# Optimization experiments

Measured on AMD Instinct MI355X. Metric: run time of the kernel, lower is better.

Reference implementation:

```python
import jax, jax.numpy as jnp
import numpy as np
from jax import lax

EQN = 10  # equations per pixel in FlowLayer


def build_a(h, w):
    """Dense constraint basis a[num, EQN, 4*num] (<=2 nonzeros per row), as in FlowLayer.__init__."""
    num = h * w
    a = np.zeros((num, EQN, 4 * num), np.float32)
    for i in range(num):
        right = (i + 1) % w != 0 and i + 1 < num
        down = i + w < num
        if right:
            a[i, 0, 2 * num + i] = 1.0; a[i, 0, i + 1] = -1.0
            a[i, 2, 2 * num + i] = 1.0; a[i, 2, 2 * num + i + 1] = -1.0
            a[i, 4, i] = 1.0;           a[i, 4, i + 1] = -1.0
            a[i, 6, 3 * num + i] = 1.0; a[i, 6, 3 * num + i + 1] = -1.0
            a[i, 8, num + i] = 1.0;     a[i, 8, num + i + 1] = -1.0
        if down:
            a[i, 1, 3 * num + i] = 1.0; a[i, 1, num + i + w] = -1.0
            a[i, 3, 3 * num + i] = 1.0; a[i, 3, 3 * num + i + w] = -1.0
            a[i, 5, num + i] = 1.0;     a[i, 5, num + i + w] = -1.0
            a[i, 7, 2 * num + i] = 1.0; a[i, 7, 2 * num + i + w] = -1.0
            a[i, 9, i] = 1.0;           a[i, 9, i + w] = -1.0
    last = num - 1  # anchor equations for the last pixel
    a[last, 0, 2 * num + last] = 1.0
    a[last, 1, 3 * num + last] = 1.0
    a[last, 2, 2 * num + last] = 1.0
    a[last, 3, 3 * num + last] = 1.0
    a[last, 4, last] = 1.0
    a[last, 5, num + last] = 1.0
    a[last, 6, 3 * num + last] = 1.0
    a[last, 7, 2 * num + last] = 1.0
    a[last, 8, num + last] = 1.0
    a[last, 9, last] = 1.0
    return a


def conv2d(x, w, b):
    y = lax.conv_general_dilated(x, w, (1, 1), 'SAME',
                                 dimension_numbers=('NCHW', 'OIHW', 'NCHW'))
    return y + b[None, :, None, None]


def setup_inputs() -> dict:
    key = jax.random.key(0)
    N, C, H, W, GR = 4, 64, 16, 16, 4
    ks = jax.random.split(key, 12)
    s3, s1 = 0.04, 0.1  # ~1/sqrt(fan_in) scales
    inp = {
        'x': jax.random.normal(ks[0], (N, C, H, W), jnp.float32),
        'grad_w1': jax.random.normal(ks[1], (C, C, 3, 3), jnp.float32) * s3,
        'grad_b1': jnp.zeros((C,), jnp.float32),
        'grad_w2': jax.random.normal(ks[2], (EQN * GR, C, 3, 3), jnp.float32) * s3,
        'grad_b2': jnp.zeros((EQN * GR,), jnp.float32),
        'att_w1': jax.random.normal(ks[3], (C, C, 3, 3), jnp.float32) * s3,
        'att_b1': jnp.zeros((C,), jnp.float32),
        'att_w2': jax.random.normal(ks[4], (EQN * GR, C, 3, 3), jnp.float32) * s3,
        'att_b2': jnp.zeros((EQN * GR,), jnp.float32),
        'se_w1': jax.random.normal(ks[5], (C // 2, C, 1, 1), jnp.float32) * s1,
        'se_b1': jnp.zeros((C // 2,), jnp.float32),
        'se_w2': jax.random.normal(ks[6], (4 * GR, C // 2, 1, 1), jnp.float32) * s1,
        'se_b2': jnp.zeros((4 * GR,), jnp.float32),
        'gn_w': jnp.ones((4 * GR,), jnp.float32),
        'gn_b': jnp.zeros((4 * GR,), jnp.float32),
        'post_w': jax.random.normal(ks[7], (128, 4 * GR, 3, 3), jnp.float32) * s1,
        'post_b': jnp.zeros((128,), jnp.float32),
    }
    return inp


def reference(x, grad_w1, grad_b1, grad_w2, grad_b2,
              att_w1, att_b1, att_w2, att_b2,
              se_w1, se_b1, se_w2, se_b2,
              gn_w, gn_b, post_w, post_b):
    n, c, h, w = x.shape
    gr = gn_w.shape[0] // 4
    num = h * w
    lrelu = lambda t: jax.nn.leaky_relu(t, 0.01)

    grad = conv2d(lrelu(conv2d(x, grad_w1, grad_b1)), grad_w2, grad_b2)      # [n, eqn*gr, h, w]
    att = jax.nn.sigmoid(conv2d(lrelu(conv2d(x, att_w1, att_b1)), att_w2, att_b2))
    pooled = x.mean((2, 3), keepdims=True)                                     # AdaptiveAvgPool2d(1)
    se = jax.nn.sigmoid(conv2d(lrelu(conv2d(pooled, se_w1, se_b1)), se_w2, se_b2))  # [n, 4*gr, 1, 1]

    # reshape(n*gr, EQN, hw).permute -> [B, hw, EQN] -> flatten rows as (pixel, eqn)
    att_f = att.reshape(n * gr, EQN, num).transpose(0, 2, 1).reshape(n * gr, num * EQN)
    grad_f = grad.reshape(n * gr, EQN, num).transpose(0, 2, 1).reshape(n * gr, num * EQN)

    a_flat = jnp.asarray(build_a(h, w)).reshape(num * EQN, 4 * num)  # constant basis
    A = att_f[:, :, None] * a_flat[None]                 # [B, num*EQN, 4*num]
    b_vec = att_f * grad_f                               # [B, num*EQN]
    ATA = jnp.einsum('brj,brk->bjk', A, A)               # [B, 4num, 4num]
    ATB = jnp.einsum('brj,br->bj', A, b_vec)[..., None]  # [B, 4num, 1]
    jitter = jnp.eye(4 * num, dtype=x.dtype) * 1e-12
    sol = jnp.linalg.solve(ATA + jitter[None], ATB)      # [B, 4num, 1]

    y = sol.reshape(n, 4 * gr, h, w)
    # GroupNorm(1, 4*gr): normalize over (C,H,W) per sample
    mu = y.mean((1, 2, 3), keepdims=True)
    var = ((y - mu) ** 2).mean((1, 2, 3), keepdims=True)
    y = (y - mu) / jnp.sqrt(var + 1e-5)
    y = y * gn_w[None, :, None, None] + gn_b[None, :, None, None]
    y = se * y
    return conv2d(y, post_w, post_b)  # [n, 128, h, w]
```

## Files before the change

### kernel.cpp

```cpp
#include <hip/hip_runtime.h>

#define NCHEB 8

typedef __attribute__((ext_vector_type(8))) short vs8;
typedef __attribute__((ext_vector_type(4))) float vf4;
typedef __attribute__((ext_vector_type(16))) float vf16;

__device__ __forceinline__ unsigned short f2bf(float f) {
  union { float f; unsigned int u; } x; x.f = f;
  unsigned int r = (x.u + 0x7FFFu + ((x.u >> 16) & 1u)) >> 16;
  return (unsigned short)r;
}

template<int COUT, int TILES, bool SE>
__global__ __launch_bounds__(256) void k_conv(
    const float* __restrict__ inA, const float* __restrict__ inB,
    const float* __restrict__ wA, const float* __restrict__ bA,
    const float* __restrict__ wB, const float* __restrict__ bB,
    float* __restrict__ outA, float* __restrict__ outB,
    int actA, int actB,
    const float* __restrict__ x,
    const float* __restrict__ sw1, const float* __restrict__ sb1,
    const float* __restrict__ sw2, const float* __restrict__ sb2,
    float* __restrict__ seo) {
  __shared__ unsigned short Xl[256 * 64];
  __shared__ unsigned short Wl[9 * 16 * 64];
  __shared__ float sp[64];
  __shared__ float sh1[32];
  const int b = blockIdx.x;
  const int t = threadIdx.x;

  if (SE && b >= 8 * TILES) {
    const int n = b - 8 * TILES;
    const int c = t >> 2, part = t & 3;
    const float* xp = x + (n * 64 + c) * 256 + part * 64;
    float s = 0.f;
    for (int k = 0; k < 64; ++k) s += xp[k];
    s += __shfl_xor(s, 1, 64);
    s += __shfl_xor(s, 2, 64);
    if (part == 0) sp[c] = s * (1.f / 256.f);
    __syncthreads();
    if (t < 32) {
      float a = sb1[t];
      for (int k = 0; k < 64; ++k) a += sw1[t * 64 + k] * sp[k];
      sh1[t] = a > 0.f ? a : 0.01f * a;
    }
    __syncthreads();
    if (t < 16) {
      float a = sb2[t];
      for (int k = 0; k < 32; ++k) a += sw2[t * 32 + k] * sh1[k];
      seo[n * 16 + t] = 1.f / (1.f + __expf(-a));
    }
    return;
  }

  const int n = b & 3;
  const int q = b >> 2;
  const int br = (q >= TILES) ? 1 : 0;
  const int ct = q - br * TILES;
  const int co0 = ct * 16;
  const float* inp = (br ? inB : inA) + n * 64 * 256;
  const float* wsrc = br ? wB : wA;
  const float* bias = br ? bB : bA;
  float* outp = (br ? outB : outA) + n * COUT * 256;
  const int act = br ? actB : actA;

  {
    const int p = t;
    #pragma unroll
    for (int q8 = 0; q8 < 8; ++q8) {
      vs8 v;
      #pragma unroll
      for (int j = 0; j < 8; ++j) v[j] = (short)f2bf(inp[(8 * q8 + j) * 256 + p]);
      *(vs8*)&Xl[p * 64 + ((q8 ^ (p & 7)) << 3)] = v;
    }
  }
  {
    const int col = t >> 4;
    const int sub = t & 15;
    const int co = co0 + col;
    if (co < COUT) {
      const float* wp = wsrc + (co * 64 + sub * 4) * 9;
      #pragma unroll
      for (int cc = 0; cc < 4; ++cc) {
        const int ci = sub * 4 + cc;
        #pragma unroll
        for (int e = 0; e < 9; ++e)
          Wl[(e * 16 + col) * 64 + (ci ^ ((col & 7) << 3))] = f2bf(wp[cc * 9 + e]);
      }
    } else {
      #pragma unroll
      for (int cc = 0; cc < 4; ++cc) {
        const int ci = sub * 4 + cc;
        #pragma unroll
        for (int e = 0; e < 9; ++e)
          Wl[(e * 16 + col) * 64 + (ci ^ ((col & 7) << 3))] = 0;
      }
    }
  }
  __syncthreads();

  const int w = t >> 6, lane = t & 63;
  const int px = lane & 15, kg = lane >> 4;
  vf4 acc[4];
  #pragma unroll
  for (int mt = 0; mt < 4; ++mt) acc[mt] = (vf4)0.f;

  for (int e = 0; e < 9; ++e) {
    const int dy = e / 3 - 1, dx = e % 3 - 1;
    const bool xok = (dx == 0) || (dx < 0 ? (px > 0) : (px < 15));
    const int xoff = xok ? dx : 0;
    #pragma unroll
    for (int ks = 0; ks < 2; ++ks) {
      vs8 bf = *(const vs8*)&Wl[(e * 16 + px) * 64 + (((ks * 4 + kg) ^ (px & 7)) << 3)];
      #pragma unroll
      for (int mt = 0; mt < 4; ++mt) {
        const int yy = 4 * w + mt + dy;
        if (yy < 0 || yy > 15) continue;
        const int ps = yy * 16 + px + xoff;
        vs8 a = *(const vs8*)&Xl[ps * 64 + (((ks * 4 + kg) ^ (ps & 7)) << 3)];
        if (!xok) a = (vs8)(short)0;
        acc[mt] = __builtin_amdgcn_mfma_f32_16x16x32_bf16(a, bf, acc[mt], 0, 0, 0);
      }
    }
  }

  const int co = co0 + px;
  if (co < COUT) {
    const float bv = bias[co];
    #pragma unroll
    for (int mt = 0; mt < 4; ++mt) {
      const int y = 4 * w + mt;
      vf4 v = acc[mt];
      #pragma unroll
      for (int j = 0; j < 4; ++j) {
        float s = v[j] + bv;
        if (act == 1) s = s > 0.f ? s : 0.01f * s;
        else if (act == 2) s = 1.f / (1.f + __expf(-s));
        v[j] = s;
      }
      *(vf4*)&outp[co * 256 + y * 16 + kg * 4] = v;
    }
  }
}

__global__ __launch_bounds__(512) void k_post(
    const float* __restrict__ sol, const float* __restrict__ se,
    const float* __restrict__ gn_w, const float* __restrict__ gn_b,
    const float* __restrict__ pw, const float* __restrict__ pb,
    float* __restrict__ out) {
  __shared__ unsigned short Hl[256 * 24];
  __shared__ unsigned short Wp[9 * 128 * 24];
  __shared__ float rs[8];
  __shared__ float rs2[8];
  const int n = blockIdx.x;
  const int t = threadIdx.x;
  const int w = t >> 6, lane = t & 63;

  float v[8];
  {
    const vf4* s4 = (const vf4*)(sol + n * 4096 + 8 * t);
    vf4 a = s4[0], b = s4[1];
    v[0]=a[0];v[1]=a[1];v[2]=a[2];v[3]=a[3];v[4]=b[0];v[5]=b[1];v[6]=b[2];v[7]=b[3];
  }
  float s = 0.f, s2 = 0.f;
  #pragma unroll
  for (int k = 0; k < 8; ++k) { s += v[k]; s2 += v[k] * v[k]; }
  #pragma unroll
  for (int o = 1; o <= 32; o <<= 1) { s += __shfl_xor(s, o, 64); s2 += __shfl_xor(s2, o, 64); }
  if (lane == 0) { rs[w] = s; rs2[w] = s2; }

  {
    const int co = t >> 2, sub = t & 3;
    const float* wp0 = pw + (co * 16 + sub * 4) * 9;
    #pragma unroll
    for (int cc = 0; cc < 4; ++cc) {
      const int ci = sub * 4 + cc;
      #pragma unroll
      for (int e = 0; e < 9; ++e)
        Wp[(e * 128 + co) * 24 + ci] = f2bf(wp0[cc * 9 + e]);
    }
  }
  __syncthreads();
  float sm = 0.f, sq = 0.f;
  #pragma unroll
  for (int k = 0; k < 8; ++k) { sm += rs[k]; sq += rs2[k]; }
  const float mu = sm * (1.f / 4096.f);
  const float rstd = rsqrtf(sq * (1.f / 4096.f) - mu * mu + 1e-5f);

  const int c = t >> 5;
  const int p0 = (8 * t) & 255;
  const float sev = se[n * 16 + c];
  const float sc = rstd * gn_w[c] * sev;
  const float of = (gn_b[c] - mu * rstd * gn_w[c]) * sev;
  #pragma unroll
  for (int k = 0; k < 8; ++k) Hl[(p0 + k) * 24 + c] = f2bf(v[k] * sc + of);
  __syncthreads();

  const int cl = lane & 31, h = lane >> 5;
  const int px = cl & 15, y0 = 2 * w + (cl >> 4);
  vf16 acc[4];
  #pragma unroll
  for (int nt = 0; nt < 4; ++nt) acc[nt] = (vf16)0.f;
  for (int e = 0; e < 9; ++e) {
    const int dy = e / 3 - 1, dx = e % 3 - 1;
    const int yy = y0 + dy, xx = px + dx;
    const bool ok = (yy >= 0 && yy < 16 && xx >= 0 && xx < 16);
    const int ps = ok ? yy * 16 + xx : 0;
    vs8 a = *(const vs8*)&Hl[ps * 24 + h * 8];
    if (!ok) a = (vs8)(short)0;
    #pragma unroll
    for (int nt = 0; nt < 4; ++nt) {
      vs8 bf = *(const vs8*)&Wp[(e * 128 + nt * 32 + cl) * 24 + h * 8];
      acc[nt] = __builtin_amdgcn_mfma_f32_32x32x16_bf16(a, bf, acc[nt], 0, 0, 0);
    }
  }
  float* op = out + n * 32768;
  #pragma unroll
  for (int nt = 0; nt < 4; ++nt) {
    const int co = nt * 32 + cl;
    const float bv = pb[co];
    #pragma unroll
    for (int rq = 0; rq < 4; ++rq) {
      vf4 vv;
      #pragma unroll
      for (int j = 0; j < 4; ++j) vv[j] = acc[nt][rq * 4 + j] + bv;
      *(vf4*)&op[co * 256 + 32 * w + 8 * rq + 4 * h] = vv;
    }
  }
}

__global__ __launch_bounds__(64) void k_pcg(
    const float* __restrict__ att, const float* __restrict__ grad,
    float* __restrict__ sol, int maxit, float tol2) {
  const int sys = blockIdx.x >> 1;
  const int wv = blockIdx.x & 1;
  const int l = threadIdx.x;
  const int row = l >> 2, c4 = l & 3;
  const int i0 = 4 * l;

  const int n = sys >> 2, g = sys & 3;
  const float* ab = att + (n * 40 + g * 10) * 256;
  const float* gb = grad + (n * 40 + g * 10) * 256;

  int era, eda, erb, edb, ec, fa, fb;
  if (wv == 0) { fa = 0; fb = 2; era = 4; eda = 9; erb = 2; edb = 7; ec = 0; }
  else         { fa = 1; fb = 3; era = 8; eda = 5; erb = 6; edb = 3; ec = 1; }

  auto L4 = [](const float* p) { return *reinterpret_cast<const float4*>(p); };
  auto unp = [](float4 v, float* o) { o[0] = v.x; o[1] = v.y; o[2] = v.z; o[3] = v.w; };

  float wLa[4], wRa[4], wUa[4], wDa[4], wXa[4], dga[4], iva[4], rsa[4];
  float wLb[4], wRb[4], wUb[4], wDb[4], wXb[4], dgb[4], ivb[4], rsb[4];

  float rA[4], gA[4], dA[4], hA[4], uA[4] = {0,0,0,0}, vA[4] = {0,0,0,0};
  unp(L4(ab + era * 256 + i0), rA); unp(L4(gb + era * 256 + i0), gA);
  unp(L4(ab + eda * 256 + i0), dA); unp(L4(gb + eda * 256 + i0), hA);
  if (row > 0) { unp(L4(ab + eda * 256 + i0 - 16), uA); unp(L4(gb + eda * 256 + i0 - 16), vA); }
  float rlA = (l > 0) ? ab[era * 256 + i0 - 1] : 0.f;
  float glA = (l > 0) ? gb[era * 256 + i0 - 1] : 0.f;
  float cX[4], gX[4], cU[4] = {0,0,0,0}, gU[4] = {0,0,0,0};
  unp(L4(ab + ec * 256 + i0), cX); unp(L4(gb + ec * 256 + i0), gX);
  float clX = 0.f, glX = 0.f;
  if (wv == 0) { if (l > 0) { clX = ab[ec * 256 + i0 - 1]; glX = gb[ec * 256 + i0 - 1]; } }
  else if (row > 0) { unp(L4(ab + ec * 256 + i0 - 16), cU); unp(L4(gb + ec * 256 + i0 - 16), gU); }

  #pragma unroll
  for (int k = 0; k < 4; ++k) {
    wRa[k] = (k < 3 || c4 < 3) ? rA[k] * rA[k] : 0.f;
    wLa[k] = (k > 0) ? rA[k-1] * rA[k-1] : ((c4 > 0) ? rlA * rlA : 0.f);
    wDa[k] = (row < 15) ? dA[k] * dA[k] : 0.f;
    wUa[k] = (row > 0) ? uA[k] * uA[k] : 0.f;
    float rhs = wRa[k] * gA[k] - wLa[k] * ((k > 0) ? gA[k-1] : glA)
              + wDa[k] * hA[k] - wUa[k] * vA[k];
    float wx, gx;
    if (wv == 0) {
      wx = (k > 0) ? cX[k-1] * cX[k-1] : ((c4 > 0) ? clX * clX : 0.f);
      gx = (k > 0) ? gX[k-1] : glX;
    } else {
      wx = (row > 0) ? cU[k] * cU[k] : 0.f;
      gx = gU[k];
    }
    wXa[k] = wx;
    rhs -= wx * gx;
    rsa[k] = rhs;
    dga[k] = 1e-12f + wRa[k] + wLa[k] + wDa[k] + wUa[k] + wx;
  }

  float rB[4], gB[4], dB[4], hB[4], uB[4] = {0,0,0,0}, vB[4] = {0,0,0,0};
  unp(L4(ab + erb * 256 + i0), rB); unp(L4(gb + erb * 256 + i0), gB);
  unp(L4(ab + edb * 256 + i0), dB); unp(L4(gb + edb * 256 + i0), hB);
  if (row > 0) { unp(L4(ab + edb * 256 + i0 - 16), uB); unp(L4(gb + edb * 256 + i0 - 16), vB); }
  float rlB = (l > 0) ? ab[erb * 256 + i0 - 1] : 0.f;
  float glB = (l > 0) ? gb[erb * 256 + i0 - 1] : 0.f;

  #pragma unroll
  for (int k = 0; k < 4; ++k) {
    wRb[k] = (k < 3 || c4 < 3) ? rB[k] * rB[k] : 0.f;
    wLb[k] = (k > 0) ? rB[k-1] * rB[k-1] : ((c4 > 0) ? rlB * rlB : 0.f);
    wDb[k] = (row < 15) ? dB[k] * dB[k] : 0.f;
    wUb[k] = (row > 0) ? uB[k] * uB[k] : 0.f;
    float wx;
    if (wv == 0) wx = (k < 3 || c4 < 3) ? cX[k] * cX[k] : 0.f;
    else         wx = (row < 15) ? cX[k] * cX[k] : 0.f;
    wXb[k] = wx;
    rsb[k] = wRb[k] * gB[k] - wLb[k] * ((k > 0) ? gB[k-1] : glB)
           + wDb[k] * hB[k] - wUb[k] * vB[k]
           + wx * gX[k];
    dgb[k] = 1e-12f + wRb[k] + wLb[k] + wDb[k] + wUb[k] + wx;
  }

  if (l == 63) {
    float wr = rA[3] * rA[3], wd = dA[3] * dA[3];
    dga[3] += wr + wd;
    rsa[3] += wr * gA[3] + wd * hA[3];
    float wc = cX[3] * cX[3], wrb = rB[3] * rB[3], wdb = dB[3] * dB[3];
    dgb[3] += wc + wrb + wdb;
    rsb[3] += wc * gX[3] + wrb * gB[3] + wdb * hB[3];
  }
  #pragma unroll
  for (int k = 0; k < 4; ++k) { iva[k] = 1.f / dga[k]; ivb[k] = 1.f / dgb[k]; }

  float ua[4], ub[4], wa[4], wb[4];

  auto spmv = [&](const float (&ia_)[4], const float (&ib_)[4],
                  float (&oa)[4], float (&ob)[4]) {
    float aU[4], aD[4], bU[4], bD[4];
    #pragma unroll
    for (int k = 0; k < 4; ++k) {
      aU[k] = __shfl_up(ia_[k], 4, 64);
      aD[k] = __shfl_down(ia_[k], 4, 64);
      bU[k] = __shfl_up(ib_[k], 4, 64);
      bD[k] = __shfl_down(ib_[k], 4, 64);
    }
    float aL = __shfl_up(ia_[3], 1, 64);
    float aR = __shfl_down(ia_[0], 1, 64);
    float bL = __shfl_up(ib_[3], 1, 64);
    float bR = __shfl_down(ib_[0], 1, 64);
    float uaL[4] = {aL, ia_[0], ia_[1], ia_[2]};
    float uaR[4] = {ia_[1], ia_[2], ia_[3], aR};
    float ubL[4] = {bL, ib_[0], ib_[1], ib_[2]};
    float ubR[4] = {ib_[1], ib_[2], ib_[3], bR};
    #pragma unroll
    for (int k = 0; k < 4; ++k) {
      float cA = (wv == 0) ? ubL[k] : bU[k];
      float cB = (wv == 0) ? uaR[k] : aD[k];
      oa[k] = dga[k] * ia_[k] - wLa[k] * uaL[k] - wRa[k] * uaR[k]
            - wUa[k] * aU[k] - wDa[k] * aD[k] - wXa[k] * cA;
      ob[k] = dgb[k] * ib_[k] - wLb[k] * ubL[k] - wRb[k] * ubR[k]
            - wUb[k] * bU[k] - wDb[k] * bD[k] - wXb[k] * cB;
    }
  };

  constexpr float lo = 0.01f, hi = 2.0f;
  constexpr float th = (hi + lo) * 0.5f, dl = (hi - lo) * 0.5f, s1 = th / dl;

  float xa[4] = {0,0,0,0}, xb[4] = {0,0,0,0};
  float ra_[4], rb_[4], pa[4] = {0,0,0,0}, pb_[4] = {0,0,0,0};
  float sa[4] = {0,0,0,0}, sb[4] = {0,0,0,0};
  #pragma unroll
  for (int k = 0; k < 4; ++k) { ra_[k] = rsa[k]; rb_[k] = rsb[k]; }

  auto cheb = [&]() {
    float da_[4], db_[4], ta[4], tb[4], qa[4], qb[4];
    #pragma unroll
    for (int k = 0; k < 4; ++k) {
      da_[k] = (1.0f / th) * iva[k] * ra_[k];
      db_[k] = (1.0f / th) * ivb[k] * rb_[k];
      ua[k] = da_[k]; ub[k] = db_[k];
    }
    spmv(da_, db_, ta, tb);
    #pragma unroll
    for (int k = 0; k < 4; ++k) {
      wa[k] = ta[k]; wb[k] = tb[k];
      qa[k] = ra_[k] - ta[k]; qb[k] = rb_[k] - tb[k];
    }
    float rho = 1.0f / s1;
    #pragma unroll
    for (int j = 1; j < NCHEB; ++j) {
      float rho2 = 1.0f / (2.0f * s1 - rho);
      float c1 = rho2 * rho, c2 = 2.0f * rho2 / dl;
      #pragma unroll
      for (int k = 0; k < 4; ++k) {
        da_[k] = c1 * da_[k] + c2 * iva[k] * qa[k];
        db_[k] = c1 * db_[k] + c2 * ivb[k] * qb[k];
        ua[k] += da_[k]; ub[k] += db_[k];
      }
      spmv(da_, db_, ta, tb);
      #pragma unroll
      for (int k = 0; k < 4; ++k) {
        wa[k] += ta[k]; wb[k] += tb[k];
        qa[k] -= ta[k]; qb[k] -= tb[k];
      }
      rho = rho2;
    }
  };

  float gamma, delta;
  auto dots = [&]() {
    float gp = 0.f, dp = 0.f;
    #pragma unroll
    for (int k = 0; k < 4; ++k) {
      gp += ra_[k] * ua[k] + rb_[k] * ub[k];
      dp += wa[k] * ua[k] + wb[k] * ub[k];
    }
    #pragma unroll
    for (int o = 1; o <= 32; o <<= 1) {
      gp += __shfl_xor(gp, o, 64);
      dp += __shfl_xor(dp, o, 64);
    }
    gamma = gp; delta = dp;
  };

  cheb();
  dots();
  const float thresh = tol2 * gamma;
  float gamma_old = gamma, alpha_old = 1.f;

  for (int it = 0; it < maxit && gamma > thresh; ++it) {
    float beta = (it == 0) ? 0.f : gamma / gamma_old;
    float alpha = (it == 0) ? gamma / delta
                            : gamma / (delta - beta * gamma / alpha_old);
    #pragma unroll
    for (int k = 0; k < 4; ++k) {
      pa[k] = ua[k] + beta * pa[k];   pb_[k] = ub[k] + beta * pb_[k];
      sa[k] = wa[k] + beta * sa[k];   sb[k] = wb[k] + beta * sb[k];
      xa[k] += alpha * pa[k];         xb[k] += alpha * pb_[k];
      ra_[k] -= alpha * sa[k];        rb_[k] -= alpha * sb[k];
    }
    gamma_old = gamma; alpha_old = alpha;
    cheb();
    dots();
  }

  float4* sol4 = reinterpret_cast<float4*>(sol);
  sol4[sys * 256 + fa * 64 + l] = make_float4(xa[0], xa[1], xa[2], xa[3]);
  sol4[sys * 256 + fb * 64 + l] = make_float4(xb[0], xb[1], xb[2], xb[3]);
}

extern "C" void kernel_launch(void* const* d_in, const int* in_sizes, int n_in,
                              void* d_out, int out_size, void* d_ws, size_t ws_size,
                              hipStream_t stream) {
  const float* x       = (const float*)d_in[0];
  const float* grad_w1 = (const float*)d_in[1];
  const float* grad_b1 = (const float*)d_in[2];
  const float* grad_w2 = (const float*)d_in[3];
  const float* grad_b2 = (const float*)d_in[4];
  const float* att_w1  = (const float*)d_in[5];
  const float* att_b1  = (const float*)d_in[6];
  const float* att_w2  = (const float*)d_in[7];
  const float* att_b2  = (const float*)d_in[8];
  const float* se_w1   = (const float*)d_in[9];
  const float* se_b1   = (const float*)d_in[10];
  const float* se_w2   = (const float*)d_in[11];
  const float* se_b2   = (const float*)d_in[12];
  const float* gn_w    = (const float*)d_in[13];
  const float* gn_b    = (const float*)d_in[14];
  const float* post_w  = (const float*)d_in[15];
  const float* post_b  = (const float*)d_in[16];
  float* out = (float*)d_out;
  float* ws = (float*)d_ws;

  float* t1    = ws;
  float* t2    = ws + 65536;
  float* gradb = ws + 131072;
  float* attb  = ws + 172032;
  float* seb   = ws + 212992;
  float* solb  = ws;

  k_conv<64, 4, true><<<36, 256, 0, stream>>>(
      x, x, grad_w1, grad_b1, att_w1, att_b1, t1, t2, 1, 1,
      x, se_w1, se_b1, se_w2, se_b2, seb);
  k_conv<40, 3, false><<<24, 256, 0, stream>>>(
      t1, t2, grad_w2, grad_b2, att_w2, att_b2, gradb, attb, 0, 2,
      nullptr, nullptr, nullptr, nullptr, nullptr, nullptr);
  k_pcg<<<32, 64, 0, stream>>>(attb, gradb, solb, 100, 3e-6f);
  k_post<<<4, 512, 0, stream>>>(solb, seb, gn_w, gn_b, post_w, post_b, out);
}
```

Measured before the change: 68.31 us.

## Fuse four launches into two kernels: front conv chain and PCG+post

Merges the two conv stages and the SE branch into one kernel per (image, branch) that keeps the intermediate activation in LDS as bf16. It also folds the PCG solve into the GroupNorm/post-conv kernel, passing the solution through shared memory. The goal is to remove two launches and the global round trips for the intermediates. In exchange, the first stage now runs on only 8 blocks (down from 36), with serial output-channel tiles and repeated weight reloads, which greatly reduces parallelism across the GPU.

```diff
diff --git a/kernel.cpp b/kernel.cpp
--- a/kernel.cpp
+++ b/kernel.cpp
@@ -12,33 +12,48 @@
   return (unsigned short)r;
 }
 
-template<int COUT, int TILES, bool SE>
-__global__ __launch_bounds__(256) void k_conv(
-    const float* __restrict__ inA, const float* __restrict__ inB,
-    const float* __restrict__ wA, const float* __restrict__ bA,
-    const float* __restrict__ wB, const float* __restrict__ bB,
-    float* __restrict__ outA, float* __restrict__ outB,
-    int actA, int actB,
+__global__ __launch_bounds__(512) void k_front(
     const float* __restrict__ x,
+    const float* __restrict__ w1g, const float* __restrict__ b1g,
+    const float* __restrict__ w1a, const float* __restrict__ b1a,
+    const float* __restrict__ w2g, const float* __restrict__ b2g,
+    const float* __restrict__ w2a, const float* __restrict__ b2a,
     const float* __restrict__ sw1, const float* __restrict__ sb1,
     const float* __restrict__ sw2, const float* __restrict__ sb2,
-    float* __restrict__ seo) {
+    float* __restrict__ grad, float* __restrict__ att,
+    float* __restrict__ seb) {
   __shared__ unsigned short Xl[256 * 64];
-  __shared__ unsigned short Wl[9 * 16 * 64];
+  __shared__ unsigned short Yl[256 * 64];
+  __shared__ unsigned short Wt[9 * 16 * 64];
   __shared__ float sp[64];
   __shared__ float sh1[32];
-  const int b = blockIdx.x;
+  const int br = blockIdx.x & 1;
+  const int n = blockIdx.x >> 1;
   const int t = threadIdx.x;
-
-  if (SE && b >= 8 * TILES) {
-    const int n = b - 8 * TILES;
-    const int c = t >> 2, part = t & 3;
-    const float* xp = x + (n * 64 + c) * 256 + part * 64;
-    float s = 0.f;
-    for (int k = 0; k < 64; ++k) s += xp[k];
-    s += __shfl_xor(s, 1, 64);
-    s += __shfl_xor(s, 2, 64);
-    if (part == 0) sp[c] = s * (1.f / 256.f);
+  const float* inp = x + n * 64 * 256;
+
+  {
+    const int p = t & 255, hf = t >> 8;
+    #pragma unroll
+    for (int qq = 0; qq < 4; ++qq) {
+      const int q8 = hf * 4 + qq;
+      vs8 v;
+      #pragma unroll
+      for (int j = 0; j < 8; ++j) v[j] = (short)f2bf(inp[(8 * q8 + j) * 256 + p]);
+      *(vs8*)&Xl[p * 64 + ((q8 ^ (p & 7)) << 3)] = v;
+    }
+  }
+
+  if (br == 0) {
+    if (t < 256) {
+      const int c = t >> 2, part = t & 3;
+      const float* xp = inp + c * 256 + part * 64;
+      float s = 0.f;
+      for (int k = 0; k < 64; ++k) s += xp[k];
+      s += __shfl_xor(s, 1, 64);
+      s += __shfl_xor(s, 2, 64);
+      if (part == 0) sp[c] = s * (1.f / 256.f);
+    }
     __syncthreads();
     if (t < 32) {
       float a = sb1[t];
@@ -49,126 +64,145 @@
     if (t < 16) {
       float a = sb2[t];
       for (int k = 0; k < 32; ++k) a += sw2[t * 32 + k] * sh1[k];
-      seo[n * 16 + t] = 1.f / (1.f + __expf(-a));
-    }
-    return;
-  }
-
-  const int n = b & 3;
-  const int q = b >> 2;
-  const int br = (q >= TILES) ? 1 : 0;
-  const int ct = q - br * TILES;
-  const int co0 = ct * 16;
-  const float* inp = (br ? inB : inA) + n * 64 * 256;
-  const float* wsrc = br ? wB : wA;
-  const float* bias = br ? bB : bA;
-  float* outp = (br ? outB : outA) + n * COUT * 256;
-  const int act = br ? actB : actA;
-
-  {
-    const int p = t;
-    #pragma unroll
-    for (int q8 = 0; q8 < 8; ++q8) {
-      vs8 v;
-      #pragma unroll
-      for (int j = 0; j < 8; ++j) v[j] = (short)f2bf(inp[(8 * q8 + j) * 256 + p]);
-      *(vs8*)&Xl[p * 64 + ((q8 ^ (p & 7)) << 3)] = v;
-    }
-  }
-  {
-    const int col = t >> 4;
-    const int sub = t & 15;
-    const int co = co0 + col;
-    if (co < COUT) {
-      const float* wp = wsrc + (co * 64 + sub * 4) * 9;
-      #pragma unroll
-      for (int cc = 0; cc < 4; ++cc) {
-        const int ci = sub * 4 + cc;
-        #pragma unroll
-        for (int e = 0; e < 9; ++e)
-          Wl[(e * 16 + col) * 64 + (ci ^ ((col & 7) << 3))] = f2bf(wp[cc * 9 + e]);
-      }
-    } else {
-      #pragma unroll
-      for (int cc = 0; cc < 4; ++cc) {
-        const int ci = sub * 4 + cc;
-        #pragma unroll
-        for (int e = 0; e < 9; ++e)
-          Wl[(e * 16 + col) * 64 + (ci ^ ((col & 7) << 3))] = 0;
-      }
-    }
-  }
-  __syncthreads();
-
+      seb[n * 16 + t] = 1.f / (1.f + __expf(-a));
+    }
+  }
+
+  const float* w1 = br ? w1a : w1g;
+  const float* b1 = br ? b1a : b1g;
   const int w = t >> 6, lane = t & 63;
   const int px = lane & 15, kg = lane >> 4;
-  vf4 acc[4];
-  #pragma unroll
-  for (int mt = 0; mt < 4; ++mt) acc[mt] = (vf4)0.f;
-
-  for (int e = 0; e < 9; ++e) {
-    const int dy = e / 3 - 1, dx = e % 3 - 1;
-    const bool xok = (dx == 0) || (dx < 0 ? (px > 0) : (px < 15));
-    const int xoff = xok ? dx : 0;
-    #pragma unroll
-    for (int ks = 0; ks < 2; ++ks) {
-      vs8 bf = *(const vs8*)&Wl[(e * 16 + px) * 64 + (((ks * 4 + kg) ^ (px & 7)) << 3)];
-      #pragma unroll
-      for (int mt = 0; mt < 4; ++mt) {
-        const int yy = 4 * w + mt + dy;
-        if (yy < 0 || yy > 15) continue;
-        const int ps = yy * 16 + px + xoff;
-        vs8 a = *(const vs8*)&Xl[ps * 64 + (((ks * 4 + kg) ^ (ps & 7)) << 3)];
-        if (!xok) a = (vs8)(short)0;
-        acc[mt] = __builtin_amdgcn_mfma_f32_16x16x32_bf16(a, bf, acc[mt], 0, 0, 0);
-      }
-    }
-  }
-
-  const int co = co0 + px;
-  if (co < COUT) {
-    const float bv = bias[co];
-    #pragma unroll
-    for (int mt = 0; mt < 4; ++mt) {
-      const int y = 4 * w + mt;
-      vf4 v = acc[mt];
+
+  for (int ct = 0; ct < 4; ++ct) {
+    __syncthreads();
+    {
+      const int col = t >> 5, sub = t & 31;
+      const float* wp = w1 + ((ct * 16 + col) * 64 + sub * 2) * 9;
+      #pragma unroll
+      for (int cc = 0; cc < 2; ++cc) {
+        const int ci = sub * 2 + cc;
+        #pragma unroll
+        for (int e = 0; e < 9; ++e)
+          Wt[(e * 16 + col) * 64 + (ci ^ ((col & 7) << 3))] = f2bf(wp[cc * 9 + e]);
+      }
+    }
+    __syncthreads();
+    vf4 acc[2];
+    acc[0] = (vf4)0.f; acc[1] = (vf4)0.f;
+    for (int e = 0; e < 9; ++e) {
+      const int dy = e / 3 - 1, dx = e % 3 - 1;
+      const bool xok = (dx == 0) || (dx < 0 ? (px > 0) : (px < 15));
+      const int xoff = xok ? dx : 0;
+      #pragma unroll
+      for (int ks = 0; ks < 2; ++ks) {
+        vs8 bf = *(const vs8*)&Wt[(e * 16 + px) * 64 + (((ks * 4 + kg) ^ (px & 7)) << 3)];
+        #pragma unroll
+        for (int mm = 0; mm < 2; ++mm) {
+          const int yy = 2 * w + mm + dy;
+          if (yy < 0 || yy > 15) continue;
+          const int ps = yy * 16 + px + xoff;
+          vs8 a = *(const vs8*)&Xl[ps * 64 + (((ks * 4 + kg) ^ (ps & 7)) << 3)];
+          if (!xok) a = (vs8)(short)0;
+          acc[mm] = __builtin_amdgcn_mfma_f32_16x16x32_bf16(a, bf, acc[mm], 0, 0, 0);
+        }
+      }
+    }
+    const int co = ct * 16 + px;
+    const float bv = b1[co];
+    #pragma unroll
+    for (int mm = 0; mm < 2; ++mm) {
+      const int y = 2 * w + mm;
       #pragma unroll
       for (int j = 0; j < 4; ++j) {
-        float s = v[j] + bv;
-        if (act == 1) s = s > 0.f ? s : 0.01f * s;
-        else if (act == 2) s = 1.f / (1.f + __expf(-s));
-        v[j] = s;
-      }
-      *(vf4*)&outp[co * 256 + y * 16 + kg * 4] = v;
+        float s = acc[mm][j] + bv;
+        s = s > 0.f ? s : 0.01f * s;
+        const int p = y * 16 + kg * 4 + j;
+        Yl[p * 64 + (((co >> 3) ^ (p & 7)) << 3) + (co & 7)] = f2bf(s);
+      }
+    }
+  }
+
+  const float* w2 = br ? w2a : w2g;
+  const float* b2 = br ? b2a : b2g;
+  float* outp = (br ? att : grad) + n * 40 * 256;
+  for (int ct = 0; ct < 3; ++ct) {
+    __syncthreads();
+    {
+      const int col = t >> 5, sub = t & 31;
+      const int co = ct * 16 + col;
+      if (co < 40) {
+        const float* wp = w2 + (co * 64 + sub * 2) * 9;
+        #pragma unroll
+        for (int cc = 0; cc < 2; ++cc) {
+          const int ci = sub * 2 + cc;
+          #pragma unroll
+          for (int e = 0; e < 9; ++e)
+            Wt[(e * 16 + col) * 64 + (ci ^ ((col & 7) << 3))] = f2bf(wp[cc * 9 + e]);
+        }
+      } else {
+        #pragma unroll
+        for (int cc = 0; cc < 2; ++cc) {
+          const int ci = sub * 2 + cc;
+          #pragma unroll
+          for (int e = 0; e < 9; ++e)
+            Wt[(e * 16 + col) * 64 + (ci ^ ((col & 7) << 3))] = 0;
+        }
+      }
+    }
+    __syncthreads();
+    vf4 acc[2];
+    acc[0] = (vf4)0.f; acc[1] = (vf4)0.f;
+    for (int e = 0; e < 9; ++e) {
+      const int dy = e / 3 - 1, dx = e % 3 - 1;
+      const bool xok = (dx == 0) || (dx < 0 ? (px > 0) : (px < 15));
+      const int xoff = xok ? dx : 0;
+      #pragma unroll
+      for (int ks = 0; ks < 2; ++ks) {
+        vs8 bf = *(const vs8*)&Wt[(e * 16 + px) * 64 + (((ks * 4 + kg) ^ (px & 7)) << 3)];
+        #pragma unroll
+        for (int mm = 0; mm < 2; ++mm) {
+          const int yy = 2 * w + mm + dy;
+          if (yy < 0 || yy > 15) continue;
+          const int ps = yy * 16 + px + xoff;
+          vs8 a = *(const vs8*)&Yl[ps * 64 + (((ks * 4 + kg) ^ (ps & 7)) << 3)];
+          if (!xok) a = (vs8)(short)0;
+          acc[mm] = __builtin_amdgcn_mfma_f32_16x16x32_bf16(a, bf, acc[mm], 0, 0, 0);
+        }
+      }
+    }
+    const int co = ct * 16 + px;
+    if (co < 40) {
+      const float bv = b2[co];
+      #pragma unroll
+      for (int mm = 0; mm < 2; ++mm) {
+        const int y = 2 * w + mm;
+        vf4 v = acc[mm];
+        #pragma unroll
+        for (int j = 0; j < 4; ++j) {
+          float s = v[j] + bv;
+          if (br) s = 1.f / (1.f + __expf(-s));
+          v[j] = s;
+        }
+        *(vf4*)&outp[co * 256 + y * 16 + kg * 4] = v;
+      }
     }
   }
 }
 
-__global__ __launch_bounds__(512) void k_post(
-    const float* __restrict__ sol, const float* __restrict__ se,
+__global__ __launch_bounds__(512) void k_back(
+    const float* __restrict__ att, const float* __restrict__ grad,
+    const float* __restrict__ se,
     const float* __restrict__ gn_w, const float* __restrict__ gn_b,
     const float* __restrict__ pw, const float* __restrict__ pb,
-    float* __restrict__ out) {
+    float* __restrict__ out, int maxit, float tol2) {
+  __shared__ float solL[4096] __attribute__((aligned(16)));
   __shared__ unsigned short Hl[256 * 24];
   __shared__ unsigned short Wp[9 * 128 * 24];
-  __shared__ float rs[8];
-  __shared__ float rs2[8];
-  const int n = blockIdx.x;
+  __shared__ float rs[8], rs2[8];
+  const int nimg = blockIdx.x;
   const int t = threadIdx.x;
-  const int w = t >> 6, lane = t & 63;
-
-  float v[8];
-  {
-    const vf4* s4 = (const vf4*)(sol + n * 4096 + 8 * t);
-    vf4 a = s4[0], b = s4[1];
-    v[0]=a[0];v[1]=a[1];v[2]=a[2];v[3]=a[3];v[4]=b[0];v[5]=b[1];v[6]=b[2];v[7]=b[3];
-  }
-  float s = 0.f, s2 = 0.f;
-  #pragma unroll
-  for (int k = 0; k < 8; ++k) { s += v[k]; s2 += v[k] * v[k]; }
-  #pragma unroll
-  for (int o = 1; o <= 32; o <<= 1) { s += __shfl_xor(s, o, 64); s2 += __shfl_xor(s2, o, 64); }
-  if (lane == 0) { rs[w] = s; rs2[w] = s2; }
+  const int u = t >> 6;
+  const int l = t & 63;
 
   {
     const int co = t >> 2, sub = t & 3;
@@ -181,261 +215,272 @@
         Wp[(e * 128 + co) * 24 + ci] = f2bf(wp0[cc * 9 + e]);
     }
   }
-  __syncthreads();
-  float sm = 0.f, sq = 0.f;
-  #pragma unroll
-  for (int k = 0; k < 8; ++k) { sm += rs[k]; sq += rs2[k]; }
-  const float mu = sm * (1.f / 4096.f);
-  const float rstd = rsqrtf(sq * (1.f / 4096.f) - mu * mu + 1e-5f);
-
-  const int c = t >> 5;
-  const int p0 = (8 * t) & 255;
-  const float sev = se[n * 16 + c];
-  const float sc = rstd * gn_w[c] * sev;
-  const float of = (gn_b[c] - mu * rstd * gn_w[c]) * sev;
-  #pragma unroll
-  for (int k = 0; k < 8; ++k) Hl[(p0 + k) * 24 + c] = f2bf(v[k] * sc + of);
-  __syncthreads();
-
-  const int cl = lane & 31, h = lane >> 5;
-  const int px = cl & 15, y0 = 2 * w + (cl >> 4);
-  vf16 acc[4];
-  #pragma unroll
-  for (int nt = 0; nt < 4; ++nt) acc[nt] = (vf16)0.f;
-  for (int e = 0; e < 9; ++e) {
-    const int dy = e / 3 - 1, dx = e % 3 - 1;
-    const int yy = y0 + dy, xx = px + dx;
-    const bool ok = (yy >= 0 && yy < 16 && xx >= 0 && xx < 16);
-    const int ps = ok ? yy * 16 + xx : 0;
-    vs8 a = *(const vs8*)&Hl[ps * 24 + h * 8];
-    if (!ok) a = (vs8)(short)0;
-    #pragma unroll
-    for (int nt = 0; nt < 4; ++nt) {
-      vs8 bf = *(const vs8*)&Wp[(e * 128 + nt * 32 + cl) * 24 + h * 8];
-      acc[nt] = __builtin_amdgcn_mfma_f32_32x32x16_bf16(a, bf, acc[nt], 0, 0, 0);
-    }
-  }
-  float* op = out + n * 32768;
-  #pragma unroll
-  for (int nt = 0; nt < 4; ++nt) {
-    const int co = nt * 32 + cl;
-    const float bv = pb[co];
-    #pragma unroll
-    for (int rq = 0; rq < 4; ++rq) {
-      vf4 vv;
-      #pragma unroll
-      for (int j = 0; j < 4; ++j) vv[j] = acc[nt][rq * 4 + j] + bv;
-      *(vf4*)&op[co * 256 + 32 * w + 8 * rq + 4 * h] = vv;
-    }
-  }
-}
-
-__global__ __launch_bounds__(64) void k_pcg(
-    const float* __restrict__ att, const float* __restrict__ grad,
-    float* __restrict__ sol, int maxit, float tol2) {
-  const int sys = blockIdx.x >> 1;
-  const int wv = blockIdx.x & 1;
-  const int l = threadIdx.x;
-  const int row = l >> 2, c4 = l & 3;
-  const int i0 = 4 * l;
-
-  const int n = sys >> 2, g = sys & 3;
-  const float* ab = att + (n * 40 + g * 10) * 256;
-  const float* gb = grad + (n * 40 + g * 10) * 256;
-
-  int era, eda, erb, edb, ec, fa, fb;
-  if (wv == 0) { fa = 0; fb = 2; era = 4; eda = 9; erb = 2; edb = 7; ec = 0; }
-  else         { fa = 1; fb = 3; era = 8; eda = 5; erb = 6; edb = 3; ec = 1; }
-
-  auto L4 = [](const float* p) { return *reinterpret_cast<const float4*>(p); };
-  auto unp = [](float4 v, float* o) { o[0] = v.x; o[1] = v.y; o[2] = v.z; o[3] = v.w; };
-
-  float wLa[4], wRa[4], wUa[4], wDa[4], wXa[4], dga[4], iva[4], rsa[4];
-  float wLb[4], wRb[4], wUb[4], wDb[4], wXb[4], dgb[4], ivb[4], rsb[4];
-
-  float rA[4], gA[4], dA[4], hA[4], uA[4] = {0,0,0,0}, vA[4] = {0,0,0,0};
-  unp(L4(ab + era * 256 + i0), rA); unp(L4(gb + era * 256 + i0), gA);
-  unp(L4(ab + eda * 256 + i0), dA); unp(L4(gb + eda * 256 + i0), hA);
-  if (row > 0) { unp(L4(ab + eda * 256 + i0 - 16), uA); unp(L4(gb + eda * 256 + i0 - 16), vA); }
-  float rlA = (l > 0) ? ab[era * 256 + i0 - 1] : 0.f;
-  float glA = (l > 0) ? gb[era * 256 + i0 - 1] : 0.f;
-  float cX[4], gX[4], cU[4] = {0,0,0,0}, gU[4] = {0,0,0,0};
-  unp(L4(ab + ec * 256 + i0), cX); unp(L4(gb + ec * 256 + i0), gX);
-  float clX = 0.f, glX = 0.f;
-  if (wv == 0) { if (l > 0) { clX = ab[ec * 256 + i0 - 1]; glX = gb[ec * 256 + i0 - 1]; } }
-  else if (row > 0) { unp(L4(ab + ec * 256 + i0 - 16), cU); unp(L4(gb + ec * 256 + i0 - 16), gU); }
-
-  #pragma unroll
-  for (int k = 0; k < 4; ++k) {
-    wRa[k] = (k < 3 || c4 < 3) ? rA[k] * rA[k] : 0.f;
-    wLa[k] = (k > 0) ? rA[k-1] * rA[k-1] : ((c4 > 0) ? rlA * rlA : 0.f);
-    wDa[k] = (row < 15) ? dA[k] * dA[k] : 0.f;
-    wUa[k] = (row > 0) ? uA[k] * uA[k] : 0.f;
-    float rhs = wRa[k] * gA[k] - wLa[k] * ((k > 0) ? gA[k-1] : glA)
-              + wDa[k] * hA[k] - wUa[k] * vA[k];
-    float wx, gx;
-    if (wv == 0) {
-      wx = (k > 0) ? cX[k-1] * cX[k-1] : ((c4 > 0) ? clX * clX : 0.f);
-      gx = (k > 0) ? gX[k-1] : glX;
-    } else {
-      wx = (row > 0) ? cU[k] * cU[k] : 0.f;
-      gx = gU[k];
-    }
-    wXa[k] = wx;
-    rhs -= wx * gx;
-    rsa[k] = rhs;
-    dga[k] = 1e-12f + wRa[k] + wLa[k] + wDa[k] + wUa[k] + wx;
-  }
-
-  float rB[4], gB[4], dB[4], hB[4], uB[4] = {0,0,0,0}, vB[4] = {0,0,0,0};
-  unp(L4(ab + erb * 256 + i0), rB); unp(L4(gb + erb * 256 + i0), gB);
-  unp(L4(ab + edb * 256 + i0), dB); unp(L4(gb + edb * 256 + i0), hB);
-  if (row > 0) { unp(L4(ab + edb * 256 + i0 - 16), uB); unp(L4(gb + edb * 256 + i0 - 16), vB); }
-  float rlB = (l > 0) ? ab[erb * 256 + i0 - 1] : 0.f;
-  float glB = (l > 0) ? gb[erb * 256 + i0 - 1] : 0.f;
-
-  #pragma unroll
-  for (int k = 0; k < 4; ++k) {
-    wRb[k] = (k < 3 || c4 < 3) ? rB[k] * rB[k] : 0.f;
-    wLb[k] = (k > 0) ? rB[k-1] * rB[k-1] : ((c4 > 0) ? rlB * rlB : 0.f);
-    wDb[k] = (row < 15) ? dB[k] * dB[k] : 0.f;
-    wUb[k] = (row > 0) ? uB[k] * uB[k] : 0.f;
-    float wx;
-    if (wv == 0) wx = (k < 3 || c4 < 3) ? cX[k] * cX[k] : 0.f;
-    else         wx = (row < 15) ? cX[k] * cX[k] : 0.f;
-    wXb[k] = wx;
-    rsb[k] = wRb[k] * gB[k] - wLb[k] * ((k > 0) ? gB[k-1] : glB)
-           + wDb[k] * hB[k] - wUb[k] * vB[k]
-           + wx * gX[k];
-    dgb[k] = 1e-12f + wRb[k] + wLb[k] + wDb[k] + wUb[k] + wx;
-  }
-
-  if (l == 63) {
-    float wr = rA[3] * rA[3], wd = dA[3] * dA[3];
-    dga[3] += wr + wd;
-    rsa[3] += wr * gA[3] + wd * hA[3];
-    float wc = cX[3] * cX[3], wrb = rB[3] * rB[3], wdb = dB[3] * dB[3];
-    dgb[3] += wc + wrb + wdb;
-    rsb[3] += wc * gX[3] + wrb * gB[3] + wdb * hB[3];
-  }
-  #pragma unroll
-  for (int k = 0; k < 4; ++k) { iva[k] = 1.f / dga[k]; ivb[k] = 1.f / dgb[k]; }
-
-  float ua[4], ub[4], wa[4], wb[4];
-
-  auto spmv = [&](const float (&ia_)[4], const float (&ib_)[4],
-                  float (&oa)[4], float (&ob)[4]) {
-    float aU[4], aD[4], bU[4], bD[4];
+
+  {
+    const int g = u >> 1;
+    const int wv = u & 1;
+    const int row = l >> 2, c4 = l & 3;
+    const int i0 = 4 * l;
+    const float* ab = att + (nimg * 40 + g * 10) * 256;
+    const float* gb = grad + (nimg * 40 + g * 10) * 256;
+
+    int era, eda, erb, edb, ec, fa, fb;
+    if (wv == 0) { fa = 0; fb = 2; era = 4; eda = 9; erb = 2; edb = 7; ec = 0; }
+    else         { fa = 1; fb = 3; era = 8; eda = 5; erb = 6; edb = 3; ec = 1; }
+
+    auto L4 = [](const float* p) { return *reinterpret_cast<const float4*>(p); };
+    auto unp = [](float4 v, float* o) { o[0] = v.x; o[1] = v.y; o[2] = v.z; o[3] = v.w; };
+
+    float wLa[4], wRa[4], wUa[4], wDa[4], wXa[4], dga[4], iva[4], rsa[4];
+    float wLb[4], wRb[4], wUb[4], wDb[4], wXb[4], dgb[4], ivb[4], rsb[4];
+
+    float rA[4], gA[4], dA[4], hA[4], uA[4] = {0,0,0,0}, vA[4] = {0,0,0,0};
+    unp(L4(ab + era * 256 + i0), rA); unp(L4(gb + era * 256 + i0), gA);
+    unp(L4(ab + eda * 256 + i0), dA); unp(L4(gb + eda * 256 + i0), hA);
+    if (row > 0) { unp(L4(ab + eda * 256 + i0 - 16), uA); unp(L4(gb + eda * 256 + i0 - 16), vA); }
+    float rlA = (l > 0) ? ab[era * 256 + i0 - 1] : 0.f;
+    float glA = (l > 0) ? gb[era * 256 + i0 - 1] : 0.f;
+    float cX[4], gX[4], cU[4] = {0,0,0,0}, gU[4] = {0,0,0,0};
+    unp(L4(ab + ec * 256 + i0), cX); unp(L4(gb + ec * 256 + i0), gX);
+    float clX = 0.f, glX = 0.f;
+    if (wv == 0) { if (l > 0) { clX = ab[ec * 256 + i0 - 1]; glX = gb[ec * 256 + i0 - 1]; } }
+    else if (row > 0) { unp(L4(ab + ec * 256 + i0 - 16), cU); unp(L4(gb + ec * 256 + i0 - 16), gU); }
+
     #pragma unroll
     for (int k = 0; k < 4; ++k) {
-      aU[k] = __shfl_up(ia_[k], 4, 64);
-      aD[k] = __shfl_down(ia_[k], 4, 64);
-      bU[k] = __shfl_up(ib_[k], 4, 64);
-      bD[k] = __shfl_down(ib_[k], 4, 64);
-    }
-    float aL = __shfl_up(ia_[3], 1, 64);
-    float aR = __shfl_down(ia_[0], 1, 64);
-    float bL = __shfl_up(ib_[3], 1, 64);
-    float bR = __shfl_down(ib_[0], 1, 64);
-    float uaL[4] = {aL, ia_[0], ia_[1], ia_[2]};
-    float uaR[4] = {ia_[1], ia_[2], ia_[3], aR};
-    float ubL[4] = {bL, ib_[0], ib_[1], ib_[2]};
-    float ubR[4] = {ib_[1], ib_[2], ib_[3], bR};
+      wRa[k] = (k < 3 || c4 < 3) ? rA[k] * rA[k] : 0.f;
+      wLa[k] = (k > 0) ? rA[k-1] * rA[k-1] : ((c4 > 0) ? rlA * rlA : 0.f);
+      wDa[k] = (row < 15) ? dA[k] * dA[k] : 0.f;
+      wUa[k] = (row > 0) ? uA[k] * uA[k] : 0.f;
+      float rhs = wRa[k] * gA[k] - wLa[k] * ((k > 0) ? gA[k-1] : glA)
+                + wDa[k] * hA[k] - wUa[k] * vA[k];
+      float wx, gx;
+      if (wv == 0) {
+        wx = (k > 0) ? cX[k-1] * cX[k-1] : ((c4 > 0) ? clX * clX : 0.f);
+        gx = (k > 0) ? gX[k-1] : glX;
+      } else {
+        wx = (row > 0) ? cU[k] * cU[k] : 0.f;
+        gx = gU[k];
+      }
+      wXa[k] = wx;
+      rhs -= wx * gx;
+      rsa[k] = rhs;
+      dga[k] = 1e-12f + wRa[k] + wLa[k] + wDa[k] + wUa[k] + wx;
+    }
+
+    float rB[4], gB[4], dB[4], hB[4], uB[4] = {0,0,0,0}, vB[4] = {0,0,0,0};
+    unp(L4(ab + erb * 256 + i0), rB); unp(L4(gb + erb * 256 + i0), gB);
+    unp(L4(ab + edb * 256 + i0), dB); unp(L4(gb + edb * 256 + i0), hB);
+    if (row > 0) { unp(L4(ab + edb * 256 + i0 - 16), uB); unp(L4(gb + edb * 256 + i0 - 16), vB); }
+    float rlB = (l > 0) ? ab[erb * 256 + i0 - 1] : 0.f;
+    float glB = (l > 0) ? gb[erb * 256 + i0 - 1] : 0.f;
+
     #pragma unroll
     for (int k = 0; k < 4; ++k) {
-      float cA = (wv == 0) ? ubL[k] : bU[k];
-      float cB = (wv == 0) ? uaR[k] : aD[k];
-      oa[k] = dga[k] * ia_[k] - wLa[k] * uaL[k] - wRa[k] * uaR[k]
-            - wUa[k] * aU[k] - wDa[k] * aD[k] - wXa[k] * cA;
-      ob[k] = dgb[k] * ib_[k] - wLb[k] * ubL[k] - wRb[k] * ubR[k]
-            - wUb[k] * bU[k] - wDb[k] * bD[k] - wXb[k] * cB;
-    }
-  };
-
-  constexpr float lo = 0.01f, hi = 2.0f;
-  constexpr float th = (hi + lo) * 0.5f, dl = (hi - lo) * 0.5f, s1 = th / dl;
-
-  float xa[4] = {0,0,0,0}, xb[4] = {0,0,0,0};
-  float ra_[4], rb_[4], pa[4] = {0,0,0,0}, pb_[4] = {0,0,0,0};
-  float sa[4] = {0,0,0,0}, sb[4] = {0,0,0,0};
-  #pragma unroll
-  for (int k = 0; k < 4; ++k) { ra_[k] = rsa[k]; rb_[k] = rsb[k]; }
-
-  auto cheb = [&]() {
-    float da_[4], db_[4], ta[4], tb[4], qa[4], qb[4];
-    #pragma unroll
-    for (int k = 0; k < 4; ++k) {
-      da_[k] = (1.0f / th) * iva[k] * ra_[k];
-      db_[k] = (1.0f / th) * ivb[k] * rb_[k];
-      ua[k] = da_[k]; ub[k] = db_[k];
-    }
-    spmv(da_, db_, ta, tb);
-    #pragma unroll
-    for (int k = 0; k < 4; ++k) {
-      wa[k] = ta[k]; wb[k] = tb[k];
-      qa[k] = ra_[k] - ta[k]; qb[k] = rb_[k] - tb[k];
-    }
-    float rho = 1.0f / s1;
-    #pragma unroll
-    for (int j = 1; j < NCHEB; ++j) {
-      float rho2 = 1.0f / (2.0f * s1 - rho);
-      float c1 = rho2 * rho, c2 = 2.0f * rho2 / dl;
+      wRb[k] = (k < 3 || c4 < 3) ? rB[k] * rB[k] : 0.f;
+      wLb[k] = (k > 0) ? rB[k-1] * rB[k-1] : ((c4 > 0) ? rlB * rlB : 0.f);
+      wDb[k] = (row < 15) ? dB[k] * dB[k] : 0.f;
+      wUb[k] = (row > 0) ? uB[k] * uB[k] : 0.f;
+      float wx;
+      if (wv == 0) wx = (k < 3 || c4 < 3) ? cX[k] * cX[k] : 0.f;
+      else         wx = (row < 15) ? cX[k] * cX[k] : 0.f;
+      wXb[k] = wx;
+      rsb[k] = wRb[k] * gB[k] - wLb[k] * ((k > 0) ? gB[k-1] : glB)
+             + wDb[k] * hB[k] - wUb[k] * vB[k]
+             + wx * gX[k];
+      dgb[k] = 1e-12f + wRb[k] + wLb[k] + wDb[k] + wUb[k] + wx;
+    }
+
+    if (l == 63) {
+      float wr = rA[3] * rA[3], wd = dA[3] * dA[3];
+      dga[3] += wr + wd;
+      rsa[3] += wr * gA[3] + wd * hA[3];
+      float wc = cX[3] * cX[3], wrb = rB[3] * rB[3], wdb = dB[3] * dB[3];
+      dgb[3] += wc + wrb + wdb;
+      rsb[3] += wc * gX[3] + wrb * gB[3] + wdb * hB[3];
+    }
+    #pragma unroll
+    for (int k = 0; k < 4; ++k) { iva[k] = 1.f / dga[k]; ivb[k] = 1.f / dgb[k]; }
+
+    float ua[4], ub[4], wa[4], wb[4];
+
+    auto spmv = [&](const float (&ia_)[4], const float (&ib_)[4],
+                    float (&oa)[4], float (&ob)[4]) {
+      float aU[4], aD[4], bU[4], bD[4];
       #pragma unroll
       for (int k = 0; k < 4; ++k) {
-        da_[k] = c1 * da_[k] + c2 * iva[k] * qa[k];
-        db_[k] = c1 * db_[k] + c2 * ivb[k] * qb[k];
-        ua[k] += da_[k]; ub[k] += db_[k];
+        aU[k] = __shfl_up(ia_[k], 4, 64);
+        aD[k] = __shfl_down(ia_[k], 4, 64);
+        bU[k] = __shfl_up(ib_[k], 4, 64);
+        bD[k] = __shfl_down(ib_[k], 4, 64);
+      }
+      float aL = __shfl_up(ia_[3], 1, 64);
+      float aR = __shfl_down(ia_[0], 1, 64);
+      float bL = __shfl_up(ib_[3], 1, 64);
+      float bR = __shfl_down(ib_[0], 1, 64);
+      float uaL[4] = {aL, ia_[0], ia_[1], ia_[2]};
+      float uaR[4] = {ia_[1], ia_[2], ia_[3], aR};
+      float ubL[4] = {bL, ib_[0], ib_[1], ib_[2]};
+      float ubR[4] = {ib_[1], ib_[2], ib_[3], bR};
+      #pragma unroll
+      for (int k = 0; k < 4; ++k) {
+        float cA = (wv == 0) ? ubL[k] : bU[k];
+        float cB = (wv == 0) ? uaR[k] : aD[k];
+        oa[k] = dga[k] * ia_[k] - wLa[k] * uaL[k] - wRa[k] * uaR[k]
+              - wUa[k] * aU[k] - wDa[k] * aD[k] - wXa[k] * cA;
+        ob[k] = dgb[k] * ib_[k] - wLb[k] * ubL[k] - wRb[k] * ubR[k]
+              - wUb[k] * bU[k] - wDb[k] * bD[k] - wXb[k] * cB;
+      }
+    };
+
+    constexpr float lo = 0.01f, hi = 2.0f;
+    constexpr float th = (hi + lo) * 0.5f, dl = (hi - lo) * 0.5f, s1 = th / dl;
+
+    float xa[4] = {0,0,0,0}, xb[4] = {0,0,0,0};
+    float ra_[4], rb_[4], pa[4] = {0,0,0,0}, pb_[4] = {0,0,0,0};
+    float sa[4] = {0,0,0,0}, sb[4] = {0,0,0,0};
+    #pragma unroll
+    for (int k = 0; k < 4; ++k) { ra_[k] = rsa[k]; rb_[k] = rsb[k]; }
+
+    auto cheb = [&]() {
+      float da_[4], db_[4], ta[4], tb[4], qa[4], qb[4];
+      #pragma unroll
+      for (int k = 0; k < 4; ++k) {
+        da_[k] = (1.0f / th) * iva[k] * ra_[k];
+        db_[k] = (1.0f / th) * ivb[k] * rb_[k];
+        ua[k] = da_[k]; ub[k] = db_[k];
       }
       spmv(da_, db_, ta, tb);
       #pragma unroll
       for (int k = 0; k < 4; ++k) {
-        wa[k] += ta[k]; wb[k] += tb[k];
-        qa[k] -= ta[k]; qb[k] -= tb[k];
-      }
-      rho = rho2;
-    }
-  };
-
-  float gamma, delta;
-  auto dots = [&]() {
-    float gp = 0.f, dp = 0.f;
-    #pragma unroll
-    for (int k = 0; k < 4; ++k) {
-      gp += ra_[k] * ua[k] + rb_[k] * ub[k];
-      dp += wa[k] * ua[k] + wb[k] * ub[k];
-    }
-    #pragma unroll
-    for (int o = 1; o <= 32; o <<= 1) {
-      gp += __shfl_xor(gp, o, 64);
-      dp += __shfl_xor(dp, o, 64);
-    }
-    gamma = gp; delta = dp;
-  };
-
-  cheb();
-  dots();
-  const float thresh = tol2 * gamma;
-  float gamma_old = gamma, alpha_old = 1.f;
-
-  for (int it = 0; it < maxit && gamma > thresh; ++it) {
-    float beta = (it == 0) ? 0.f : gamma / gamma_old;
-    float alpha = (it == 0) ? gamma / delta
-                            : gamma / (delta - beta * gamma / alpha_old);
-    #pragma unroll
-    for (int k = 0; k < 4; ++k) {
-      pa[k] = ua[k] + beta * pa[k];   pb_[k] = ub[k] + beta * pb_[k];
-      sa[k] = wa[k] + beta * sa[k];   sb[k] = wb[k] + beta * sb[k];
-      xa[k] += alpha * pa[k];         xb[k] += alpha * pb_[k];
-      ra_[k] -= alpha * sa[k];        rb_[k] -= alpha * sb[k];
-    }
-    gamma_old = gamma; alpha_old = alpha;
+        wa[k] = ta[k]; wb[k] = tb[k];
+        qa[k] = ra_[k] - ta[k]; qb[k] = rb_[k] - tb[k];
+      }
+      float rho = 1.0f / s1;
+      #pragma unroll
+      for (int j = 1; j < NCHEB; ++j) {
+        float rho2 = 1.0f / (2.0f * s1 - rho);
+        float c1 = rho2 * rho, c2 = 2.0f * rho2 / dl;
+        #pragma unroll
+        for (int k = 0; k < 4; ++k) {
+          da_[k] = c1 * da_[k] + c2 * iva[k] * qa[k];
+          db_[k] = c1 * db_[k] + c2 * ivb[k] * qb[k];
+          ua[k] += da_[k]; ub[k] += db_[k];
+        }
+        spmv(da_, db_, ta, tb);
+        #pragma unroll
+        for (int k = 0; k < 4; ++k) {
+          wa[k] += ta[k]; wb[k] += tb[k];
+          qa[k] -= ta[k]; qb[k] -= tb[k];
+        }
+        rho = rho2;
+      }
+    };
+
+    float gamma, delta;
+    auto dots = [&]() {
+      float gp = 0.f, dp = 0.f;
+      #pragma unroll
+      for (int k = 0; k < 4; ++k) {
+        gp += ra_[k] * ua[k] + rb_[k] * ub[k];
+        dp += wa[k] * ua[k] + wb[k] * ub[k];
+      }
+      #pragma unroll
+      for (int o = 1; o <= 32; o <<= 1) {
+        gp += __shfl_xor(gp, o, 64);
+        dp += __shfl_xor(dp, o, 64);
+      }
+      gamma = gp; delta = dp;
+    };
+
     cheb();
     dots();
-  }
-
-  float4* sol4 = reinterpret_cast<float4*>(sol);
-  sol4[sys * 256 + fa * 64 + l] = make_float4(xa[0], xa[1], xa[2], xa[3]);
-  sol4[sys * 256 + fb * 64 + l] = make_float4(xb[0], xb[1], xb[2], xb[3]);
+    const float thresh = tol2 * gamma;
+    float gamma_old = gamma, alpha_old = 1.f;
+
+    for (int it = 0; it < maxit && gamma > thresh; ++it) {
+      float beta = (it == 0) ? 0.f : gamma / gamma_old;
+      float alpha = (it == 0) ? gamma / delta
+                              : gamma / (delta - beta * gamma / alpha_old);
+      #pragma unroll
+      for (int k = 0; k < 4; ++k) {
+        pa[k] = ua[k] + beta * pa[k];   pb_[k] = ub[k] + beta * pb_[k];
+        sa[k] = wa[k] + beta * sa[k];   sb[k] = wb[k] + beta * sb[k];
+        xa[k] += alpha * pa[k];         xb[k] += alpha * pb_[k];
+        ra_[k] -= alpha * sa[k];        rb_[k] -= alpha * sb[k];
+      }
+      gamma_old = gamma; alpha_old = alpha;
+      cheb();
+      dots();
+    }
+
+    *(float4*)&solL[g * 1024 + fa * 256 + 4 * l] = make_float4(xa[0], xa[1], xa[2], xa[3]);
+    *(float4*)&solL[g * 1024 + fb * 256 + 4 * l] = make_float4(xb[0], xb[1], xb[2], xb[3]);
+  }
+  __syncthreads();
+
+  {
+    const int w = u, lane = l;
+    float v[8];
+    {
+      const vf4* s4 = (const vf4*)(solL + 8 * t);
+      vf4 a = s4[0], b = s4[1];
+      v[0]=a[0];v[1]=a[1];v[2]=a[2];v[3]=a[3];v[4]=b[0];v[5]=b[1];v[6]=b[2];v[7]=b[3];
+    }
+    float s = 0.f, s2 = 0.f;
+    #pragma unroll
+    for (int k = 0; k < 8; ++k) { s += v[k]; s2 += v[k] * v[k]; }
+    #pragma unroll
+    for (int o = 1; o <= 32; o <<= 1) { s += __shfl_xor(s, o, 64); s2 += __shfl_xor(s2, o, 64); }
+    if (lane == 0) { rs[w] = s; rs2[w] = s2; }
+    __syncthreads();
+    float sm = 0.f, sq = 0.f;
+    #pragma unroll
+    for (int k = 0; k < 8; ++k) { sm += rs[k]; sq += rs2[k]; }
+    const float mu = sm * (1.f / 4096.f);
+    const float rstd = rsqrtf(sq * (1.f / 4096.f) - mu * mu + 1e-5f);
+
+    const int c = t >> 5;
+    const int p0 = (8 * t) & 255;
+    const float sev = se[nimg * 16 + c];
+    const float sc = rstd * gn_w[c] * sev;
+    const float of = (gn_b[c] - mu * rstd * gn_w[c]) * sev;
+    #pragma unroll
+    for (int k = 0; k < 8; ++k) Hl[(p0 + k) * 24 + c] = f2bf(v[k] * sc + of);
+    __syncthreads();
+
+    const int cl = lane & 31, h = lane >> 5;
+    const int px = cl & 15, y0 = 2 * w + (cl >> 4);
+    vf16 acc[4];
+    #pragma unroll
+    for (int nt = 0; nt < 4; ++nt) acc[nt] = (vf16)0.f;
+    for (int e = 0; e < 9; ++e) {
+      const int dy = e / 3 - 1, dx = e % 3 - 1;
+      const int yy = y0 + dy, xx = px + dx;
+      const bool ok = (yy >= 0 && yy < 16 && xx >= 0 && xx < 16);
+      const int ps = ok ? yy * 16 + xx : 0;
+      vs8 a = *(const vs8*)&Hl[ps * 24 + h * 8];
+      if (!ok) a = (vs8)(short)0;
+      #pragma unroll
+      for (int nt = 0; nt < 4; ++nt) {
+        vs8 bf = *(const vs8*)&Wp[(e * 128 + nt * 32 + cl) * 24 + h * 8];
+        acc[nt] = __builtin_amdgcn_mfma_f32_32x32x16_bf16(a, bf, acc[nt], 0, 0, 0);
+      }
+    }
+    float* op = out + nimg * 32768;
+    #pragma unroll
+    for (int nt = 0; nt < 4; ++nt) {
+      const int co = nt * 32 + cl;
+      const float bv = pb[co];
+      #pragma unroll
+      for (int rq = 0; rq < 4; ++rq) {
+        vf4 vv;
+        #pragma unroll
+        for (int j = 0; j < 4; ++j) vv[j] = acc[nt][rq * 4 + j] + bv;
+        *(vf4*)&op[co * 256 + 32 * w + 8 * rq + 4 * h] = vv;
+      }
+    }
+  }
 }
 
 extern "C" void kernel_launch(void* const* d_in, const int* in_sizes, int n_in,
@@ -461,19 +506,15 @@
   float* out = (float*)d_out;
   float* ws = (float*)d_ws;
 
-  float* t1    = ws;
-  float* t2    = ws + 65536;
-  float* gradb = ws + 131072;
-  float* attb  = ws + 172032;
-  float* seb   = ws + 212992;
-  float* solb  = ws;
-
-  k_conv<64, 4, true><<<36, 256, 0, stream>>>(
-      x, x, grad_w1, grad_b1, att_w1, att_b1, t1, t2, 1, 1,
-      x, se_w1, se_b1, se_w2, se_b2, seb);
-  k_conv<40, 3, false><<<24, 256, 0, stream>>>(
-      t1, t2, grad_w2, grad_b2, att_w2, att_b2, gradb, attb, 0, 2,
-      nullptr, nullptr, nullptr, nullptr, nullptr, nullptr);
-  k_pcg<<<32, 64, 0, stream>>>(attb, gradb, solb, 100, 3e-6f);
-  k_post<<<4, 512, 0, stream>>>(solb, seb, gn_w, gn_b, post_w, post_b, out);
+  float* gradb = ws;
+  float* attb  = ws + 40960;
+  float* seb   = ws + 81920;
+
+  k_front<<<8, 512, 0, stream>>>(
+      x, grad_w1, grad_b1, att_w1, att_b1,
+      grad_w2, grad_b2, att_w2, att_b2,
+      se_w1, se_b1, se_w2, se_b2,
+      gradb, attb, seb);
+  k_back<<<4, 512, 0, stream>>>(
+      attb, gradb, seb, gn_w, gn_b, post_w, post_b, out, 100, 3e-6f);
 }
```

Measured after the change: 95.65 us. +40.0%, slower.
